# Kernel optimization log

Hardware: AMD Instinct MI355X
Metric: run time of the kernel (lower is better)

The kernel has to match this reference:

```python
import jax, jax.numpy as jnp
import numpy as np
from jax import lax

K = 3            # RFAConv kernel size
CIN = 66         # RFAConv in_channel = c2/2 + 2
UP = 64          # up channel count = c2/2
BN_EPS = 1e-5


def conv2d(x, w, stride=1, padding=0, groups=1, bias=None):
    out = lax.conv_general_dilated(
        x, w, (stride, stride), [(padding, padding), (padding, padding)],
        dimension_numbers=("NCHW", "OIHW", "NCHW"), feature_group_count=groups)
    if bias is not None:
        out = out + bias[None, :, None, None]
    return out


def avgpool3(x):
    # AvgPool2d(kernel=3, pad=1, stride=1), count_include_pad=True -> /9 everywhere
    s = lax.reduce_window(x, 0.0, lax.add, (1, 1, 3, 3), (1, 1, 1, 1),
                          [(0, 0), (0, 0), (1, 1), (1, 1)])
    return s / 9.0


def setup_inputs() -> dict:
    key = jax.random.key(0)
    ks = jax.random.split(key, 8)
    c1, c2 = 64, 128
    inp = {
        "x": jax.random.normal(ks[0], (8, c1, 256, 256), jnp.float32),
        "w_squeeze": jax.random.normal(ks[1], (c2, 4 * c1, 1, 1), jnp.float32) * 0.05,
        "w_gw": jax.random.normal(ks[2], (CIN * K * K, 1, 1, 1), jnp.float32) * 0.3,
        "w_gf": jax.random.normal(ks[3], (CIN * K * K, 1, K, K), jnp.float32) * 0.3,
        "bn_gamma": jnp.ones((CIN * K * K,), jnp.float32),
        "bn_beta": jnp.zeros((CIN * K * K,), jnp.float32),
        "bn_mean": jnp.zeros((CIN * K * K,), jnp.float32),
        "bn_var": jnp.ones((CIN * K * K,), jnp.float32),
        "w_conv": jax.random.normal(ks[4], (UP, CIN, K, K), jnp.float32) * 0.05,
        "b_conv": jnp.zeros((UP,), jnp.float32),
    }
    return inp


def reference(x, w_squeeze, w_gw, w_gf, bn_gamma, bn_beta, bn_mean, bn_var,
              w_conv, b_conv):
    # space_to_depth: [B,C,H,W] -> [B,4C,H/2,W/2]
    x = jnp.concatenate([x[..., ::2, ::2], x[..., 1::2, ::2],
                         x[..., ::2, 1::2], x[..., 1::2, 1::2]], axis=1)
    # squeeze0: 1x1 conv 4*c1 -> c2
    x = conv2d(x, w_squeeze)
    up, low = x[:, :UP], x[:, UP:]

    # AddCoords (with_r=False): append normalized xx (width) and yy (height)
    b, _, h, w = up.shape
    xx = (jnp.arange(w, dtype=up.dtype) / (w - 1) * 2.0 - 1.0)
    yy = (jnp.arange(h, dtype=up.dtype) / (h - 1) * 2.0 - 1.0)
    xx = jnp.broadcast_to(xx[None, None, None, :], (b, 1, h, w))
    yy = jnp.broadcast_to(yy[None, None, :, None], (b, 1, h, w))
    up = jnp.concatenate([up, xx, yy], axis=1)   # [b, 66, h, w]

    # RFAConv
    weight = conv2d(avgpool3(up), w_gw, groups=CIN)          # [b, 594, h, w]
    weight = jax.nn.softmax(weight.reshape(b, CIN, K * K, h, w), axis=2)

    feat = conv2d(up, w_gf, stride=1, padding=1, groups=CIN)  # [b, 594, h, w]
    scale = bn_gamma / jnp.sqrt(bn_var + BN_EPS)
    shift = bn_beta - bn_mean * scale
    feat = jax.nn.relu(feat * scale[None, :, None, None] + shift[None, :, None, None])
    feat = feat.reshape(b, CIN, K * K, h, w)

    wd = feat * weight
    # rearrange 'b c (n1 n2) h w -> b c (h n1) (w n2)'
    wd = wd.reshape(b, CIN, K, K, h, w).transpose(0, 1, 4, 2, 5, 3)
    wd = wd.reshape(b, CIN, h * K, w * K)
    up = conv2d(wd, w_conv, stride=K, bias=b_conv)            # [b, 64, h, w]

    y = jnp.concatenate([up, low], axis=1)                    # [b, 128, h, w]
    # channel shuffle: gather even channels then odd channels
    bb, n, hh, ww = y.shape
    y = y.reshape(bb, n // 2, 2, hh, ww)
    return jnp.concatenate([y[:, :, 0], y[:, :, 1]], axis=1)
```

## Files before the change

kernel.cpp:

```cpp
#include <hip/hip_runtime.h>
#include <math.h>

typedef __attribute__((ext_vector_type(8))) short short8;
typedef __attribute__((ext_vector_type(4))) float f32x4;

#define CIN 66
#define BN_EPS 1e-5f

#define PLROW 136
#define PLN   17680

#define CO_F     ((size_t)4587520)
#define BSQ_U16  ((size_t)16777216)
#define BSQ_CNT  32768
#define BF_U16   (BSQ_U16 + BSQ_CNT)
#define BF_CNT   36864
#define SC_F     ((size_t)8424448)
#define SH_F     (SC_F + 594)

static __device__ __forceinline__ unsigned short f2bf(float f) {
    unsigned u = __float_as_uint(f);
    u += 0x7fffu + ((u >> 16) & 1u);
    return (unsigned short)(u >> 16);
}
static __device__ __forceinline__ unsigned pack2(float lo, float hi) {
    return __builtin_amdgcn_perm(__float_as_uint(hi) + 0x8000u,
                                 __float_as_uint(lo) + 0x8000u, 0x07060302u);
}

__global__ void prep_kernel(const float* __restrict__ w_squeeze,
                            const float* __restrict__ gamma,
                            const float* __restrict__ beta,
                            const float* __restrict__ mean,
                            const float* __restrict__ var,
                            const float* __restrict__ w_gw,
                            const float* __restrict__ w_gf,
                            const float* __restrict__ w_conv,
                            float* __restrict__ ws)
{
    unsigned short* wsu = (unsigned short*)ws;
    const int tid = blockIdx.x * blockDim.x + threadIdx.x;
    const int nth = gridDim.x * blockDim.x;

    for (int idx = tid; idx < BSQ_CNT; idx += nth) {
        int j = idx & 7, lane = (idx >> 3) & 63, r = idx >> 9;
        int nt = r & 7, kc = r >> 3;
        int k = kc * 32 + ((lane >> 4) << 3) + j;
        int n = nt * 16 + (lane & 15);
        wsu[BSQ_U16 + idx] = f2bf(w_squeeze[n * 256 + k]);
    }
    for (int idx = tid; idx < BF_CNT; idx += nth) {
        int j = idx & 7, lane = (idx >> 3) & 63, r = idx >> 9;
        int nt = r & 3, ks = r >> 2;
        int k = ks * 32 + ((lane >> 4) << 3) + j;
        int n = nt * 16 + (lane & 15);
        wsu[BF_U16 + idx] = f2bf(w_conv[n * 594 + k]);
    }
    for (int i = tid; i < CIN * 9; i += nth) {
        float sc = gamma[i] / sqrtf(var[i] + BN_EPS);
        ws[SC_F + i] = sc;
        ws[SH_F + i] = beta[i] - mean[i] * sc;
    }
    for (int idx = tid; idx < 512 * 648; idx += nth) {
        int plane = idx / 648, r = idx - plane * 648;
        unsigned* pb = (unsigned*)(wsu + (size_t)plane * PLN);
        if (r < 68)       pb[r] = 0u;
        else if (r < 136) pb[8772 + (r - 68)] = 0u;
        else {
            int rr = (r - 136) >> 2, k = (r - 136) & 3;
            pb[(rr + 1) * 68 + (k < 2 ? k : 64 + k)] = 0u;
        }
    }
    if (tid < 65536) {
        const int pix = tid & 16383;
        const int g   = tid >> 14;
        const int h = pix >> 7, w = pix & 127;
        float fsA[9], fsB[9];
#pragma unroll
        for (int c = 0; c < 2; ++c) {
            const int cu = 64 + c;
            float n[9];
#pragma unroll
            for (int dy = 0; dy < 3; ++dy)
#pragma unroll
                for (int dx = 0; dx < 3; ++dx) {
                    const int gy = h - 1 + dy, gx = w - 1 + dx;
                    const bool ok = ((unsigned)gy < 128u) & ((unsigned)gx < 128u);
                    const float v = (c == 0) ? (gx * (2.f / 127.f) - 1.f)
                                             : (gy * (2.f / 127.f) - 1.f);
                    n[dy * 3 + dx] = ok ? v : 0.f;
                }
            const float p = (n[0]+n[1]+n[2]+n[3]+n[4]+n[5]+n[6]+n[7]+n[8]) * (1.f/9.f);
            const float* gw = w_gw + cu * 9;
            const float* gf = w_gf + cu * 81;
            float e[9], se = 0.f;
#pragma unroll
            for (int j = 0; j < 9; ++j) { e[j] = __expf(p * gw[j]); se += e[j]; }
            const float sinv = 1.f / se;
            float* fs = c ? fsB : fsA;
#pragma unroll
            for (int j = 0; j < 9; ++j) {
                float cv = 0.f;
#pragma unroll
                for (int i = 0; i < 9; ++i) cv = fmaf(n[i], gf[j * 9 + i], cv);
                const float sc = gamma[cu * 9 + j] / sqrtf(var[cu * 9 + j] + BN_EPS);
                const float sh = beta[cu * 9 + j] - mean[cu * 9 + j] * sc;
                const float f = fmaf(cv, sc, sh);
                fs[j] = fmaxf(f, 0.f) * (e[j] * sinv);
            }
        }
#pragma unroll 1
        for (int oc = g * 16; oc < g * 16 + 16; ++oc) {
            const float* wc = w_conv + oc * 594;
            float s = 0.f;
#pragma unroll
            for (int j = 0; j < 9; ++j)
                s = fmaf(fsA[j], wc[576 + j], fmaf(fsB[j], wc[585 + j], s));
            ws[CO_F + (size_t)oc * 16384 + pix] = s;
        }
    }
}

__global__ __launch_bounds__(256, 4) void squeeze_mfma(
    const float* __restrict__ x,
    float* __restrict__ wsp,
    float* __restrict__ out)
{
    __shared__ uint4 As[32 * 64];

    const int bx  = blockIdx.x;
    const int b   = bx & 7;
    const int pos = bx >> 3;
    const int h   = pos >> 1;
    const int w0  = (pos & 1) * 64;
    const int tid  = threadIdx.x;
    const int lane = tid & 63;
    const int wv   = tid >> 6;
    const int oct = tid >> 5;
    const int pp  = tid & 31;

    float4 v[2][8];
#pragma unroll
    for (int gy = 0; gy < 2; ++gy)
#pragma unroll
        for (int i = 0; i < 8; ++i)
            v[gy][i] = *(const float4*)(x +
                (size_t)(b * 64 + oct * 8 + i) * 65536 +
                (2 * h + gy) * 256 + 2 * w0 + 4 * pp);

#pragma unroll
    for (int gy = 0; gy < 2; ++gy)
#pragma unroll
        for (int gx = 0; gx < 2; ++gx)
#pragma unroll
            for (int p = 0; p < 2; ++p) {
                const int comp = p * 2 + gx;
                uint4 u;
                u.x = pack2(((const float*)&v[gy][0])[comp], ((const float*)&v[gy][1])[comp]);
                u.y = pack2(((const float*)&v[gy][2])[comp], ((const float*)&v[gy][3])[comp]);
                u.z = pack2(((const float*)&v[gy][4])[comp], ((const float*)&v[gy][5])[comp]);
                u.w = pack2(((const float*)&v[gy][6])[comp], ((const float*)&v[gy][7])[comp]);
                As[((gy + 2 * gx) * 8 + oct) * 64 + 2 * pp + p] = u;
            }

    const unsigned short* bsq = (const unsigned short*)wsp + BSQ_U16;
    short8 b0 = *(const short8*)(bsq + (size_t)((2 * wv + 0) * 64 + lane) * 8);
    short8 b1 = *(const short8*)(bsq + (size_t)((2 * wv + 1) * 64 + lane) * 8);

    __syncthreads();

    const int q = lane >> 4, m = lane & 15;
    f32x4 acc[4][2];
#pragma unroll
    for (int mt = 0; mt < 4; ++mt)
#pragma unroll
        for (int j = 0; j < 2; ++j) acc[mt][j] = (f32x4){0.f, 0.f, 0.f, 0.f};

#pragma unroll
    for (int ks = 0; ks < 8; ++ks) {
        short8 nb0, nb1;
        if (ks < 7) {
            nb0 = *(const short8*)(bsq + (size_t)(((ks + 1) * 8 + 2 * wv + 0) * 64 + lane) * 8);
            nb1 = *(const short8*)(bsq + (size_t)(((ks + 1) * 8 + 2 * wv + 1) * 64 + lane) * 8);
        }
#pragma unroll
        for (int mt = 0; mt < 4; ++mt) {
            short8 a = *(const short8*)&As[(ks * 4 + q) * 64 + mt * 16 + m];
            acc[mt][0] = __builtin_amdgcn_mfma_f32_16x16x32_bf16(a, b0, acc[mt][0], 0, 0, 0);
            acc[mt][1] = __builtin_amdgcn_mfma_f32_16x16x32_bf16(a, b1, acc[mt][1], 0, 0, 0);
        }
        if (ks < 7) { b0 = nb0; b1 = nb1; }
    }

    if (wv < 2) {
        unsigned short* upw = (unsigned short*)wsp;
#pragma unroll
        for (int j = 0; j < 2; ++j) {
            const int oc = (2 * wv + j) * 16 + m;
#pragma unroll
            for (int mt = 0; mt < 4; ++mt) {
                uint2 st;
                st.x = pack2(acc[mt][j][0], acc[mt][j][1]);
                st.y = pack2(acc[mt][j][2], acc[mt][j][3]);
                *(uint2*)(upw + (size_t)(b * 64 + oc) * PLN + (size_t)(h + 1) * PLROW
                          + (w0 + mt * 16 + q * 4 + 4)) = st;
            }
        }
    } else {
#pragma unroll
        for (int j = 0; j < 2; ++j) {
            const int oc = (2 * wv + j) * 16 + m;
            const int lc = oc - 64;
            const int ch = (lc & 1) ? (96 + ((lc - 1) >> 1)) : (32 + (lc >> 1));
#pragma unroll
            for (int mt = 0; mt < 4; ++mt) {
                float4 st = {acc[mt][j][0], acc[mt][j][1], acc[mt][j][2], acc[mt][j][3]};
                *(float4*)(out + ((size_t)(b * 128 + ch) * 128 + h) * 128
                           + (w0 + mt * 16 + q * 4)) = st;
            }
        }
    }
}

__device__ __forceinline__ void fs_from_n(
    int cu, const float n[9],
    const float* __restrict__ w_gw, const float* __restrict__ w_gf,
    const float* __restrict__ scp, const float* __restrict__ shp,
    float fs[9])
{
    const float p = (n[0] + n[1] + n[2] + n[3] + n[4] + n[5] + n[6] + n[7] + n[8]) * (1.f / 9.f);
    const float* gw = w_gw + cu * 9;
    const float* gf = w_gf + cu * 81;
    const float* sc = scp + cu * 9;
    const float* sh = shp + cu * 9;
    float e[9], se = 0.f;
#pragma unroll
    for (int j = 0; j < 9; ++j) { e[j] = __expf(p * gw[j]); se += e[j]; }
    const float sinv = 1.f / se;
#pragma unroll
    for (int j = 0; j < 9; ++j) {
        float cv = n[0] * gf[j * 9 + 0];
        cv = fmaf(n[1], gf[j * 9 + 1], cv); cv = fmaf(n[2], gf[j * 9 + 2], cv);
        cv = fmaf(n[3], gf[j * 9 + 3], cv); cv = fmaf(n[4], gf[j * 9 + 4], cv);
        cv = fmaf(n[5], gf[j * 9 + 5], cv); cv = fmaf(n[6], gf[j * 9 + 6], cv);
        cv = fmaf(n[7], gf[j * 9 + 7], cv); cv = fmaf(n[8], gf[j * 9 + 8], cv);
        float f = fmaf(cv, sc[j], sh[j]);
        fs[j] = fmaxf(f, 0.f) * (e[j] * sinv);
    }
}

__device__ __forceinline__ void pack_into(unsigned* pk, int ci, const float fs[9], float& carry)
{
    const int off = 9 * ci;
    if ((ci & 1) == 0) {
#pragma unroll
        for (int t = 0; t < 4; ++t) pk[off / 2 + t] = pack2(fs[2 * t], fs[2 * t + 1]);
        carry = fs[8];
    } else {
        pk[(off - 1) / 2] = pack2(carry, fs[0]);
#pragma unroll
        for (int t = 0; t < 4; ++t) pk[(off + 1) / 2 + t] = pack2(fs[1 + 2 * t], fs[2 + 2 * t]);
    }
}

__device__ __forceinline__ void chunk_loads(
    int cbase, int lane, int h0, int w0,
    const unsigned short* __restrict__ upb, uint2 vr[8][3])
{
    const int px = lane & 7, py = lane >> 3;
    const size_t rowoff = (size_t)(h0 + py) * PLROW + (size_t)((w0 + px + 3) & ~1);
#pragma unroll
    for (int ci = 0; ci < 8; ++ci) {
        const int cu = __builtin_amdgcn_readfirstlane(cbase + ci);
        const unsigned short* cb = upb + (size_t)cu * PLN + rowoff;
#pragma unroll
        for (int dy = 0; dy < 3; ++dy)
            vr[ci][dy] = *(const uint2*)(cb + dy * PLROW);
    }
}

__device__ __forceinline__ void chunk_compute(
    int cbase, int lane, const uint2 vr[8][3],
    const float* __restrict__ w_gw, const float* __restrict__ w_gf,
    const float* __restrict__ scp, const float* __restrict__ shp,
    unsigned pk[36])
{
    const unsigned sh = (lane & 1) ? 0u : 16u;
    float carry = 0.f;
#pragma unroll
    for (int ci = 0; ci < 8; ++ci) {
        const int cu = __builtin_amdgcn_readfirstlane(cbase + ci);
        float n[9];
#pragma unroll
        for (int dy = 0; dy < 3; ++dy) {
            const uint2 vv = vr[ci][dy];
            unsigned long long t = (((unsigned long long)vv.y) << 32) | vv.x;
            t >>= sh;
            n[dy * 3 + 0] = __uint_as_float((unsigned)t << 16);
            n[dy * 3 + 1] = __uint_as_float((unsigned)t & 0xffff0000u);
            n[dy * 3 + 2] = __uint_as_float((unsigned)(t >> 32) << 16);
        }
        float fs[9];
        fs_from_n(cu, n, w_gw, w_gf, scp, shp, fs);
        pack_into(pk, ci, fs, carry);
    }
}

template<int NSTEPS>
__device__ __forceinline__ void do_mfma(
    int base, const uint4* As, const unsigned short* __restrict__ bfw,
    int wv, int lane, f32x4 acc[2][2])
{
    const int q = lane >> 4, m = lane & 15;
    const int ntb = (wv >> 1) * 2;
    const int pt0 = (wv & 1) * 2;
#pragma unroll
    for (int ks = 0; ks < NSTEPS; ++ks) {
        short8 b0 = *(const short8*)(bfw + (size_t)(((base + ks) * 4 + ntb + 0) * 64 + lane) * 8);
        short8 b1 = *(const short8*)(bfw + (size_t)(((base + ks) * 4 + ntb + 1) * 64 + lane) * 8);
#pragma unroll
        for (int mt = 0; mt < 2; ++mt) {
            short8 a = *(const short8*)&As[(ks * 4 + q) * 64 + (pt0 + mt) * 16 + m];
            acc[mt][0] = __builtin_amdgcn_mfma_f32_16x16x32_bf16(a, b0, acc[mt][0], 0, 0, 0);
            acc[mt][1] = __builtin_amdgcn_mfma_f32_16x16x32_bf16(a, b1, acc[mt][1], 0, 0, 0);
        }
    }
}

__global__ __launch_bounds__(256, 4) void fused_mfma(
    const float* __restrict__ wsp,
    const float* __restrict__ w_gw,
    const float* __restrict__ w_gf,
    const float* __restrict__ b_conv,
    float* __restrict__ out)
{
    __shared__ uint4 As[36 * 64];

    const int bx = blockIdx.x;
    const int b  = bx & 7;
    const int t  = bx >> 3;
    const int w0 = (t & 15) * 8;
    const int h0 = ((t >> 4) & 15) * 8;
    const int tid = threadIdx.x, lane = tid & 63, wv = tid >> 6;

    const unsigned short* upb = (const unsigned short*)wsp + (size_t)b * 64 * PLN;
    const float* scp = wsp + SC_F;
    const float* shp = wsp + SH_F;
    const unsigned short* bfw = (const unsigned short*)wsp + BF_U16;

    f32x4 acc[2][2];
#pragma unroll
    for (int mt = 0; mt < 2; ++mt)
#pragma unroll
        for (int j = 0; j < 2; ++j) acc[mt][j] = (f32x4){0.f, 0.f, 0.f, 0.f};

    uint2 vr[8][3];
    unsigned pk[36];

    chunk_loads(8 * wv, lane, h0, w0, upb, vr);
    chunk_compute(8 * wv, lane, vr, w_gw, w_gf, scp, shp, pk);
#pragma unroll
    for (int kb = 0; kb < 9; ++kb)
        As[(9 * wv + kb) * 64 + lane] =
            (uint4){pk[4 * kb], pk[4 * kb + 1], pk[4 * kb + 2], pk[4 * kb + 3]};
    __syncthreads();

    chunk_loads(32 + 8 * wv, lane, h0, w0, upb, vr);
    do_mfma<9>(0, As, bfw, wv, lane, acc);
    chunk_compute(32 + 8 * wv, lane, vr, w_gw, w_gf, scp, shp, pk);
    __syncthreads();
#pragma unroll
    for (int kb = 0; kb < 9; ++kb)
        As[(9 * wv + kb) * 64 + lane] =
            (uint4){pk[4 * kb], pk[4 * kb + 1], pk[4 * kb + 2], pk[4 * kb + 3]};
    __syncthreads();
    do_mfma<9>(9, As, bfw, wv, lane, acc);

    const int q = lane >> 4, m = lane & 15;
    const int ntb = (wv >> 1) * 2, pt0 = (wv & 1) * 2;
    const float* co = wsp + CO_F;
#pragma unroll
    for (int mt = 0; mt < 2; ++mt)
#pragma unroll
        for (int j = 0; j < 2; ++j) {
            const int oc = (ntb + j) * 16 + m;
            const int ch = (oc & 1) ? (64 + (oc >> 1)) : (oc >> 1);
            const int row = h0 + (pt0 + mt) * 2 + (q >> 1);
            const int col = w0 + (q & 1) * 4;
            const size_t pix = (size_t)row * 128 + col;
            const float4 cv = *(const float4*)(co + (size_t)oc * 16384 + pix);
            const float bias = b_conv[oc];
            float4 st = { acc[mt][j][0] + bias + cv.x,
                          acc[mt][j][1] + bias + cv.y,
                          acc[mt][j][2] + bias + cv.z,
                          acc[mt][j][3] + bias + cv.w };
            *(float4*)(out + (size_t)(b * 128 + ch) * 16384 + pix) = st;
        }
}

extern "C" void kernel_launch(void* const* d_in, const int* in_sizes, int n_in,
                              void* d_out, int out_size, void* d_ws, size_t ws_size,
                              hipStream_t stream)
{
    const float* x         = (const float*)d_in[0];
    const float* w_squeeze = (const float*)d_in[1];
    const float* w_gw      = (const float*)d_in[2];
    const float* w_gf      = (const float*)d_in[3];
    const float* gamma     = (const float*)d_in[4];
    const float* beta      = (const float*)d_in[5];
    const float* mean      = (const float*)d_in[6];
    const float* var       = (const float*)d_in[7];
    const float* w_conv    = (const float*)d_in[8];
    const float* b_conv    = (const float*)d_in[9];
    float* out = (float*)d_out;
    float* ws  = (float*)d_ws;

    prep_kernel<<<256, 256, 0, stream>>>(w_squeeze, gamma, beta, mean, var,
                                         w_gw, w_gf, w_conv, ws);
    squeeze_mfma<<<2048, 256, 0, stream>>>(x, ws, out);
    fused_mfma<<<2048, 256, 0, stream>>>(ws, w_gw, w_gf, b_conv, out);
}
```

Baseline: 334.1 us.

## Split fused RFA stage into four smaller channel chunks and prefold BN/softmax constants

```diff
diff --git a/kernel.cpp b/kernel.cpp
--- a/kernel.cpp
+++ b/kernel.cpp
@@ -14,9 +14,11 @@
 #define BSQ_U16  ((size_t)16777216)
 #define BSQ_CNT  32768
 #define BF_U16   (BSQ_U16 + BSQ_CNT)
-#define BF_CNT   36864
-#define SC_F     ((size_t)8424448)
+#define BF_CNT   40960
+#define SC_F     ((size_t)8425472)
 #define SH_F     (SC_F + 594)
+#define GW2_F    (SH_F + 594)
+#define GF2_F    (GW2_F + 594)
 
 static __device__ __forceinline__ unsigned short f2bf(float f) {
     unsigned u = __float_as_uint(f);
@@ -52,14 +54,25 @@
     for (int idx = tid; idx < BF_CNT; idx += nth) {
         int j = idx & 7, lane = (idx >> 3) & 63, r = idx >> 9;
         int nt = r & 3, ks = r >> 2;
-        int k = ks * 32 + ((lane >> 4) << 3) + j;
+        int kp = ks * 32 + ((lane >> 4) << 3) + j;
+        int chunk = kp / 160, rem = kp - chunk * 160;
+        int wvv = rem / 40, s = rem - wvv * 40;
         int n = nt * 16 + (lane & 15);
-        wsu[BF_U16 + idx] = f2bf(w_conv[n * 594 + k]);
+        float v = 0.f;
+        if (s < 36) v = w_conv[n * 594 + chunk * 144 + wvv * 36 + s];
+        wsu[BF_U16 + idx] = f2bf(v);
     }
     for (int i = tid; i < CIN * 9; i += nth) {
         float sc = gamma[i] / sqrtf(var[i] + BN_EPS);
         ws[SC_F + i] = sc;
         ws[SH_F + i] = beta[i] - mean[i] * sc;
+    }
+    for (int i = tid; i < CIN * 9; i += nth)
+        ws[GW2_F + i] = w_gw[i] * 0.16029944573f;
+    for (int i = tid; i < CIN * 81; i += nth) {
+        int cj = i / 9;
+        float sc = gamma[cj] * rsqrtf(var[cj] + BN_EPS);
+        ws[GF2_F + i] = w_gf[i] * sc;
     }
     for (int idx = tid; idx < 512 * 648; idx += nth) {
         int plane = idx / 648, r = idx - plane * 648;
@@ -222,30 +235,25 @@
     }
 }
 
-__device__ __forceinline__ void fs_from_n(
+__device__ __forceinline__ void fs_from_n2(
     int cu, const float n[9],
-    const float* __restrict__ w_gw, const float* __restrict__ w_gf,
-    const float* __restrict__ scp, const float* __restrict__ shp,
-    float fs[9])
-{
-    const float p = (n[0] + n[1] + n[2] + n[3] + n[4] + n[5] + n[6] + n[7] + n[8]) * (1.f / 9.f);
-    const float* gw = w_gw + cu * 9;
-    const float* gf = w_gf + cu * 81;
-    const float* sc = scp + cu * 9;
+    const float* __restrict__ gw2, const float* __restrict__ gf2,
+    const float* __restrict__ shp, float fs[9])
+{
+    const float s = ((n[0] + n[1]) + (n[2] + n[3])) + ((n[4] + n[5]) + (n[6] + n[7])) + n[8];
+    const float* gw = gw2 + cu * 9;
+    const float* gf = gf2 + cu * 81;
     const float* sh = shp + cu * 9;
     float e[9], se = 0.f;
 #pragma unroll
-    for (int j = 0; j < 9; ++j) { e[j] = __expf(p * gw[j]); se += e[j]; }
-    const float sinv = 1.f / se;
+    for (int j = 0; j < 9; ++j) { e[j] = __builtin_amdgcn_exp2f(s * gw[j]); se += e[j]; }
+    const float sinv = __builtin_amdgcn_rcpf(se);
 #pragma unroll
     for (int j = 0; j < 9; ++j) {
-        float cv = n[0] * gf[j * 9 + 0];
-        cv = fmaf(n[1], gf[j * 9 + 1], cv); cv = fmaf(n[2], gf[j * 9 + 2], cv);
-        cv = fmaf(n[3], gf[j * 9 + 3], cv); cv = fmaf(n[4], gf[j * 9 + 4], cv);
-        cv = fmaf(n[5], gf[j * 9 + 5], cv); cv = fmaf(n[6], gf[j * 9 + 6], cv);
-        cv = fmaf(n[7], gf[j * 9 + 7], cv); cv = fmaf(n[8], gf[j * 9 + 8], cv);
-        float f = fmaf(cv, sc[j], sh[j]);
-        fs[j] = fmaxf(f, 0.f) * (e[j] * sinv);
+        float cv = sh[j];
+#pragma unroll
+        for (int i = 0; i < 9; ++i) cv = fmaf(n[i], gf[j * 9 + i], cv);
+        fs[j] = fmaxf(cv, 0.f) * (e[j] * sinv);
     }
 }
 
@@ -263,14 +271,14 @@
     }
 }
 
-__device__ __forceinline__ void chunk_loads(
+__device__ __forceinline__ void chunk_loads4(
     int cbase, int lane, int h0, int w0,
-    const unsigned short* __restrict__ upb, uint2 vr[8][3])
+    const unsigned short* __restrict__ upb, uint2 vr[4][3])
 {
     const int px = lane & 7, py = lane >> 3;
     const size_t rowoff = (size_t)(h0 + py) * PLROW + (size_t)((w0 + px + 3) & ~1);
 #pragma unroll
-    for (int ci = 0; ci < 8; ++ci) {
+    for (int ci = 0; ci < 4; ++ci) {
         const int cu = __builtin_amdgcn_readfirstlane(cbase + ci);
         const unsigned short* cb = upb + (size_t)cu * PLN + rowoff;
 #pragma unroll
@@ -279,45 +287,44 @@
     }
 }
 
-__device__ __forceinline__ void chunk_compute(
-    int cbase, int lane, const uint2 vr[8][3],
-    const float* __restrict__ w_gw, const float* __restrict__ w_gf,
-    const float* __restrict__ scp, const float* __restrict__ shp,
-    unsigned pk[36])
-{
-    const unsigned sh = (lane & 1) ? 0u : 16u;
+__device__ __forceinline__ void chunk_compute4(
+    int cbase, int lane, const uint2 vr[4][3],
+    const float* __restrict__ gw2, const float* __restrict__ gf2,
+    const float* __restrict__ shp, unsigned pk[20])
+{
+    const unsigned shf = (lane & 1) ? 0u : 16u;
     float carry = 0.f;
 #pragma unroll
-    for (int ci = 0; ci < 8; ++ci) {
+    for (int ci = 0; ci < 4; ++ci) {
         const int cu = __builtin_amdgcn_readfirstlane(cbase + ci);
         float n[9];
 #pragma unroll
         for (int dy = 0; dy < 3; ++dy) {
             const uint2 vv = vr[ci][dy];
             unsigned long long t = (((unsigned long long)vv.y) << 32) | vv.x;
-            t >>= sh;
+            t >>= shf;
             n[dy * 3 + 0] = __uint_as_float((unsigned)t << 16);
             n[dy * 3 + 1] = __uint_as_float((unsigned)t & 0xffff0000u);
             n[dy * 3 + 2] = __uint_as_float((unsigned)(t >> 32) << 16);
         }
         float fs[9];
-        fs_from_n(cu, n, w_gw, w_gf, scp, shp, fs);
+        fs_from_n2(cu, n, gw2, gf2, shp, fs);
         pack_into(pk, ci, fs, carry);
     }
-}
-
-template<int NSTEPS>
-__device__ __forceinline__ void do_mfma(
-    int base, const uint4* As, const unsigned short* __restrict__ bfw,
+    pk[18] = 0u; pk[19] = 0u;
+}
+
+__device__ __forceinline__ void do_mfma5(
+    int bbase, const uint4* As, const unsigned short* __restrict__ bfw,
     int wv, int lane, f32x4 acc[2][2])
 {
     const int q = lane >> 4, m = lane & 15;
     const int ntb = (wv >> 1) * 2;
     const int pt0 = (wv & 1) * 2;
 #pragma unroll
-    for (int ks = 0; ks < NSTEPS; ++ks) {
-        short8 b0 = *(const short8*)(bfw + (size_t)(((base + ks) * 4 + ntb + 0) * 64 + lane) * 8);
-        short8 b1 = *(const short8*)(bfw + (size_t)(((base + ks) * 4 + ntb + 1) * 64 + lane) * 8);
+    for (int ks = 0; ks < 5; ++ks) {
+        short8 b0 = *(const short8*)(bfw + (size_t)(((bbase + ks) * 4 + ntb + 0) * 64 + lane) * 8);
+        short8 b1 = *(const short8*)(bfw + (size_t)(((bbase + ks) * 4 + ntb + 1) * 64 + lane) * 8);
 #pragma unroll
         for (int mt = 0; mt < 2; ++mt) {
             short8 a = *(const short8*)&As[(ks * 4 + q) * 64 + (pt0 + mt) * 16 + m];
@@ -327,14 +334,12 @@
     }
 }
 
-__global__ __launch_bounds__(256, 4) void fused_mfma(
+__global__ __launch_bounds__(256, 6) void fused_mfma(
     const float* __restrict__ wsp,
-    const float* __restrict__ w_gw,
-    const float* __restrict__ w_gf,
     const float* __restrict__ b_conv,
     float* __restrict__ out)
 {
-    __shared__ uint4 As[36 * 64];
+    __shared__ uint4 As[20 * 64];
 
     const int bx = blockIdx.x;
     const int b  = bx & 7;
@@ -344,7 +349,8 @@
     const int tid = threadIdx.x, lane = tid & 63, wv = tid >> 6;
 
     const unsigned short* upb = (const unsigned short*)wsp + (size_t)b * 64 * PLN;
-    const float* scp = wsp + SC_F;
+    const float* gw2 = wsp + GW2_F;
+    const float* gf2 = wsp + GF2_F;
     const float* shp = wsp + SH_F;
     const unsigned short* bfw = (const unsigned short*)wsp + BF_U16;
 
@@ -354,27 +360,31 @@
 #pragma unroll
         for (int j = 0; j < 2; ++j) acc[mt][j] = (f32x4){0.f, 0.f, 0.f, 0.f};
 
-    uint2 vr[8][3];
-    unsigned pk[36];
-
-    chunk_loads(8 * wv, lane, h0, w0, upb, vr);
-    chunk_compute(8 * wv, lane, vr, w_gw, w_gf, scp, shp, pk);
-#pragma unroll
-    for (int kb = 0; kb < 9; ++kb)
-        As[(9 * wv + kb) * 64 + lane] =
+    uint2 vr[4][3];
+    unsigned pk[20];
+
+    chunk_loads4(wv * 4, lane, h0, w0, upb, vr);
+    chunk_compute4(wv * 4, lane, vr, gw2, gf2, shp, pk);
+#pragma unroll
+    for (int kb = 0; kb < 5; ++kb)
+        As[(5 * wv + kb) * 64 + lane] =
             (uint4){pk[4 * kb], pk[4 * kb + 1], pk[4 * kb + 2], pk[4 * kb + 3]};
     __syncthreads();
 
-    chunk_loads(32 + 8 * wv, lane, h0, w0, upb, vr);
-    do_mfma<9>(0, As, bfw, wv, lane, acc);
-    chunk_compute(32 + 8 * wv, lane, vr, w_gw, w_gf, scp, shp, pk);
-    __syncthreads();
-#pragma unroll
-    for (int kb = 0; kb < 9; ++kb)
-        As[(9 * wv + kb) * 64 + lane] =
-            (uint4){pk[4 * kb], pk[4 * kb + 1], pk[4 * kb + 2], pk[4 * kb + 3]};
-    __syncthreads();
-    do_mfma<9>(9, As, bfw, wv, lane, acc);
+#pragma unroll
+    for (int c = 0; c < 4; ++c) {
+        if (c < 3) chunk_loads4((c + 1) * 16 + wv * 4, lane, h0, w0, upb, vr);
+        do_mfma5(c * 5, As, bfw, wv, lane, acc);
+        if (c < 3) {
+            chunk_compute4((c + 1) * 16 + wv * 4, lane, vr, gw2, gf2, shp, pk);
+            __syncthreads();
+#pragma unroll
+            for (int kb = 0; kb < 5; ++kb)
+                As[(5 * wv + kb) * 64 + lane] =
+                    (uint4){pk[4 * kb], pk[4 * kb + 1], pk[4 * kb + 2], pk[4 * kb + 3]};
+            __syncthreads();
+        }
+    }
 
     const int q = lane >> 4, m = lane & 15;
     const int ntb = (wv >> 1) * 2, pt0 = (wv & 1) * 2;
@@ -418,5 +428,5 @@
     prep_kernel<<<256, 256, 0, stream>>>(w_squeeze, gamma, beta, mean, var,
                                          w_gw, w_gf, w_conv, ws);
     squeeze_mfma<<<2048, 256, 0, stream>>>(x, ws, out);
-    fused_mfma<<<2048, 256, 0, stream>>>(ws, w_gw, w_gf, b_conv, out);
-}
+    fused_mfma<<<2048, 256, 0, stream>>>(ws, b_conv, out);
+}
```

Result: faster. 318.6 us (-4.6%).
